# Performance work log

Measured on AMD Instinct MI355X. Metric: run time of the kernel, lower is better.

The kernel has to match this reference:

```python
import jax, jax.numpy as jnp
import numpy as np

N, E, H, C = 100000, 1600000, 64, 40

def _mlp(h, w1, b1, w2, b2):
    return jax.nn.relu(h @ w1 + b1) @ w2 + b2

def setup_inputs() -> dict:
    key = jax.random.key(0)
    ks = jax.random.split(key, 16)
    def w(k, shape, fan_in):
        return jax.random.normal(k, shape, jnp.float32) / np.sqrt(fan_in)
    return {
        "x": jax.random.normal(ks[0], (N, H), jnp.float32),
        "edge_index": jax.random.randint(ks[1], (2, E), 0, N, jnp.int64),
        "edge_attr": jax.random.normal(ks[2], (E, 1), jnp.float32),
        # edge_mlp: Linear(1,H) -> ReLU -> Linear(H,H)
        "e_w1": w(ks[3], (1, H), 1), "e_b1": jnp.zeros((H,), jnp.float32),
        "e_w2": w(ks[4], (H, H), H), "e_b2": jnp.zeros((H,), jnp.float32),
        # conv1 update MLP + eps
        "eps1": jnp.zeros((), jnp.float32),
        "m1_w1": w(ks[5], (H, H), H), "m1_b1": jnp.zeros((H,), jnp.float32),
        "m1_w2": w(ks[6], (H, H), H), "m1_b2": jnp.zeros((H,), jnp.float32),
        # conv2 update MLP + eps
        "eps2": jnp.zeros((), jnp.float32),
        "m2_w1": w(ks[7], (H, H), H), "m2_b1": jnp.zeros((H,), jnp.float32),
        "m2_w2": w(ks[8], (H, H), H), "m2_b2": jnp.zeros((H,), jnp.float32),
        # classifier
        "lin_w": w(ks[9], (H, C), H), "lin_b": jnp.zeros((C,), jnp.float32),
    }

def reference(x, edge_index, edge_attr, e_w1, e_b1, e_w2, e_b2,
              eps1, m1_w1, m1_b1, m1_w2, m1_b2,
              eps2, m2_w1, m2_b1, m2_w2, m2_b2, lin_w, lin_b):
    n = x.shape[0]
    src, dst = edge_index[0], edge_index[1]
    edge_emb = _mlp(edge_attr, e_w1, e_b1, e_w2, e_b2)  # [E, H]

    def gine_conv(h, eps, w1, b1, w2, b2):
        msg = jax.nn.relu(h[src] + edge_emb)                 # gather + fuse  [E, H]
        aggr = jax.ops.segment_sum(msg, dst, num_segments=n) # scatter-add   [N, H]
        return _mlp((1.0 + eps) * h + aggr, w1, b1, w2, b2)

    h = jax.nn.relu(gine_conv(x, eps1, m1_w1, m1_b1, m1_w2, m1_b2))
    # dropout is identity in eval mode
    h = jax.nn.relu(gine_conv(h, eps2, m2_w1, m2_b1, m2_w2, m2_b2))
    return jax.nn.log_softmax(h @ lin_w + lin_b, axis=1)
```

## Files before the change

### kernel.cpp

```cpp
#include <hip/hip_runtime.h>
#include <hip/hip_bf16.h>
#include <stdint.h>


typedef unsigned int uint32;
typedef unsigned short ushort16;
typedef __attribute__((ext_vector_type(8))) short bf16x8;
typedef __attribute__((ext_vector_type(4))) float f32x4;

#define BKT_SHIFT 9
#define BKT_SIZE 512
#define BKT_MASK 511
#define BSPLIT 4

static __device__ __forceinline__ unsigned short f2bf(float f) {
  __hip_bfloat16 h = __float2bfloat16(f);
  return *reinterpret_cast<unsigned short*>(&h);
}
static __device__ __forceinline__ float bf2f(unsigned short u) {
  return __uint_as_float(((uint32)u) << 16);
}

static __device__ __forceinline__ bool detect_is64(const uint32* ei, int E, int tid, int* sflag) {
  if (tid < 64) {
    int lim = (E < 64) ? E : 64;
    int nz = (tid < lim) ? (ei[2 * (size_t)tid + 1] != 0u) : 0;
    nz = __any(nz);
    if (tid == 0) *sflag = !nz;
  }
  __syncthreads();
  return *sflag != 0;
}

__global__ __launch_bounds__(256) void k_setup_cast_count(
    const float* __restrict__ w1, const float* __restrict__ b1,
    const float* __restrict__ w2, const float* __restrict__ b2,
    float* __restrict__ tsS, float2* __restrict__ ABp,
    const float* __restrict__ xin, ushort16* __restrict__ xb, int n4,
    const uint32* __restrict__ ei, int* __restrict__ hist1, int E, int KB) {
  __shared__ float w2s[64 * 64];
  __shared__ float b2s[64];
  __shared__ float w1s[64], b1s[64], ts[64];
  __shared__ int rs[64], ms[64], vs[64];
  __shared__ int h[1024];
  __shared__ int sIs64;
  const int tid = threadIdx.x;
  const int CB = (n4 + 255) >> 8;
  if (blockIdx.x >= (uint32)(65 + CB)) {
    const int b = blockIdx.x - (65 + CB);
    for (int i = tid; i < 1024; i += 256) h[i] = 0;
    bool is64 = detect_is64(ei, E, tid, &sIs64);
    for (int i = b * 256 + tid; i < E; i += KB * 256) {
      int dst = is64 ? (int)ei[2 * ((size_t)E + i)] : (int)ei[(size_t)E + i];
      atomicAdd(&h[dst >> BKT_SHIFT], 1);
    }
    __syncthreads();
    for (int i = tid; i < 1024; i += 256)
      if (h[i]) atomicAdd(&hist1[i], h[i]);
    return;
  }
  if (blockIdx.x >= 65) {
    int i = (blockIdx.x - 65) * 256 + tid;
    if (i < n4) {
      float4 v = ((const float4*)xin)[i];
      ushort4 o;
      o.x = f2bf(v.x); o.y = f2bf(v.y); o.z = f2bf(v.z); o.w = f2bf(v.w);
      ((ushort4*)xb)[i] = o;
    }
    return;
  }
  const int p = blockIdx.x;
  {
    const float4* g4 = (const float4*)w2;
    float4* s4 = (float4*)w2s;
    for (int i = tid; i < 64 * 16; i += 256) s4[i] = g4[i];
    if (tid < 64) b2s[tid] = b2[tid];
  }
  if (tid < 64) {
    float w = w1[tid], b = b1[tid];
    w1s[tid] = w; b1s[tid] = b;
    int v = (w != 0.0f);
    vs[tid] = v;
    ts[tid] = v ? (-b / w) : 0.0f;
  }
  __syncthreads();
  if (tid < 64) {
    float tk = ts[tid];
    int r = 0, m = 0;
    for (int k = 0; k < 64; ++k) if (vs[k]) { r += (ts[k] < tk) ? 1 : 0; m += (ts[k] == tk) ? 1 : 0; }
    rs[tid] = r; ms[tid] = m;
    if (p == 0) {
      int pos;
      if (vs[tid]) {
        int c = 0;
        for (int j = 0; j < 64; ++j)
          if (vs[j] && (ts[j] < tk || (ts[j] == tk && j < tid))) c++;
        pos = c;
      } else {
        int c = 0;
        for (int j = 0; j < 64; ++j) if (vs[j]) c++;
        for (int j = 0; j < tid; ++j) if (!vs[j]) c++;
        pos = c;
      }
      tsS[pos] = vs[tid] ? tk : __builtin_inff();
    }
  }
  __syncthreads();
  if (tid < 64) {
    const int j = tid;
    float accA = 0.0f, accB = b2s[j];
    for (int k = 0; k < 64; ++k) {
      bool act;
      if (vs[k]) act = (w1s[k] > 0.0f) ? (p >= rs[k] + ms[k]) : (p <= rs[k]);
      else       act = (b1s[k] > 0.0f);
      if (act) { float wv = w2s[k * 64 + j]; accA = fmaf(w1s[k], wv, accA); accB = fmaf(b1s[k], wv, accB); }
    }
    ABp[p * 64 + j] = make_float2(accA, accB);
  }
}

static __device__ __forceinline__ int scan_hist(const int* __restrict__ hist1,
                                                int* bo, int* psum, int tid) {
  int v0 = hist1[tid * 4 + 0], v1 = hist1[tid * 4 + 1];
  int v2 = hist1[tid * 4 + 2], v3 = hist1[tid * 4 + 3];
  int sum = v0 + v1 + v2 + v3;
  psum[tid] = sum;
  __syncthreads();
  for (int d = 1; d < 256; d <<= 1) {
    int add = (tid >= d) ? psum[tid - d] : 0;
    __syncthreads();
    psum[tid] += add;
    __syncthreads();
  }
  int run = psum[tid] - sum;
  bo[tid * 4 + 0] = run; run += v0;
  bo[tid * 4 + 1] = run; run += v1;
  bo[tid * 4 + 2] = run; run += v2;
  bo[tid * 4 + 3] = run; run += v3;
  int total = psum[255];
  __syncthreads();
  return total;
}

__global__ __launch_bounds__(256) void k_bpart(
    const uint32* __restrict__ ei, const float* __restrict__ ea,
    const float* __restrict__ tsSg, const int* __restrict__ hist1,
    int* __restrict__ bCur,
    int2* __restrict__ stage, unsigned short* __restrict__ dstw, int E) {
  __shared__ int cnt[1024];
  __shared__ int bo[1024];
  __shared__ int psum[256];
  __shared__ float tss[64];
  __shared__ int sIs64;
  __shared__ int2 sspay[2048];
  __shared__ uint32 ssmeta[2048];
  const int tid = threadIdx.x;
  for (int i = tid; i < 1024; i += 256) cnt[i] = 0;
  if (tid >= 64 && tid < 128) tss[tid - 64] = tsSg[tid - 64];
  bool is64 = detect_is64(ei, E, tid, &sIs64);
  scan_hist(hist1, bo, psum, tid);
  const int base0 = blockIdx.x * 2048;
  int dstv[8], srcv[8], rk[8];
  float av[8];
#pragma unroll
  for (int e = 0; e < 8; ++e) {
    int idx = base0 + e * 256 + tid;
    if (idx < E) {
      int src, dst;
      if (is64) { src = (int)ei[2 * (size_t)idx]; dst = (int)ei[2 * ((size_t)E + idx)]; }
      else      { src = (int)ei[(size_t)idx];     dst = (int)ei[(size_t)E + idx]; }
      dstv[e] = dst; srcv[e] = src; av[e] = ea[idx];
      rk[e] = atomicAdd(&cnt[dst >> BKT_SHIFT], 1);
    } else dstv[e] = -1;
  }
  __syncthreads();
  for (int b = tid; b < 1024; b += 256) {
    int c = cnt[b];
    if (c) bo[b] = bo[b] + atomicAdd(&bCur[b], c);
  }
  int v0 = cnt[tid * 4 + 0], v1 = cnt[tid * 4 + 1];
  int v2 = cnt[tid * 4 + 2], v3 = cnt[tid * 4 + 3];
  int lsum = v0 + v1 + v2 + v3;
  __syncthreads();
  psum[tid] = lsum;
  __syncthreads();
  for (int d = 1; d < 256; d <<= 1) {
    int add = (tid >= d) ? psum[tid - d] : 0;
    __syncthreads();
    psum[tid] += add;
    __syncthreads();
  }
  int lrun = psum[tid] - lsum;
  cnt[tid * 4 + 0] = lrun; lrun += v0;
  cnt[tid * 4 + 1] = lrun; lrun += v1;
  cnt[tid * 4 + 2] = lrun; lrun += v2;
  cnt[tid * 4 + 3] = lrun;
  const int totloc = psum[255];
  __syncthreads();
#pragma unroll
  for (int e = 0; e < 8; ++e) {
    if (dstv[e] < 0) continue;
    float a = av[e];
    int p = 0;
#pragma unroll
    for (int s = 32; s > 0; s >>= 1) if (tss[p + s - 1] < a) p += s;
    if (tss[p] < a) ++p;
    const int b = dstv[e] >> BKT_SHIFT;
    const int slot = cnt[b] + rk[e];
    const int gd = bo[b] + rk[e];
    sspay[slot] = make_int2(srcv[e] | (p << 20), __float_as_int(a));
    ssmeta[slot] = (uint32)gd | ((uint32)(dstv[e] & BKT_MASK) << 21);
  }
  __syncthreads();
  for (int j = tid; j < totloc; j += 256) {
    uint32 m = ssmeta[j];
    int gd = (int)(m & 0x1FFFFFu);
    stage[gd] = sspay[j];
    dstw[gd] = (unsigned short)(m >> 21);
  }
}

__global__ __launch_bounds__(256) void k_blocal(
    const int* __restrict__ hist1, const int2* __restrict__ stage,
    const unsigned short* __restrict__ dstw,
    int* __restrict__ offs, int2* __restrict__ pay, int N) {
  __shared__ int bo[1024];
  __shared__ int psum[256];
  __shared__ int h[512], cur[512], ps2[256];
  const int tid = threadIdx.x;
  const int b = blockIdx.x >> 2;
  const int sub = blockIdx.x & 3;
  const int nbkt = (int)gridDim.x >> 2;
  int Etot = scan_hist(hist1, bo, psum, tid);
  const int s = bo[b];
  const int e2 = (b == nbkt - 1) ? Etot : bo[b + 1];
  if (b == 0 && sub == 0 && tid == 0) offs[N] = Etot;
  h[tid] = 0; h[tid + 256] = 0;
  __syncthreads();
  for (int j = s + tid; j < e2; j += 256) atomicAdd(&h[dstw[j]], 1);
  __syncthreads();
  int a0 = h[2 * tid], a1 = h[2 * tid + 1];
  ps2[tid] = a0 + a1;
  __syncthreads();
  for (int d = 1; d < 256; d <<= 1) {
    int add = (tid >= d) ? ps2[tid - d] : 0;
    __syncthreads();
    ps2[tid] += add;
    __syncthreads();
  }
  int ex = s + ps2[tid] - (a0 + a1);
  cur[2 * tid] = ex;
  cur[2 * tid + 1] = ex + a0;
  {
    int local = 2 * tid;
    if ((local >> 7) == sub) {
      int nd0 = b * BKT_SIZE + local;
      if (nd0 < N) offs[nd0] = ex;
      if (nd0 + 1 < N) offs[nd0 + 1] = ex + a0;
    }
  }
  __syncthreads();
  const int lo = sub << 7, hi = lo + 128;
  for (int j = s + tid; j < e2; j += 256) {
    int d = dstw[j];
    if (d >= lo && d < hi) {
      int pos = atomicAdd(&cur[d], 1);
      pay[pos] = stage[j];
    }
  }
}

#define EDGE8_LOAD(ib, qx, av)                                   \
  _Pragma("unroll")                                              \
  for (int t = 0; t < 8; ++t) {                                  \
    int2 q_ = pay[(ib) + t];                                     \
    qx[t] = (uint32)__builtin_amdgcn_readfirstlane(q_.x);        \
    av[t] = __uint_as_float((uint32)__builtin_amdgcn_readfirstlane(q_.y)); \
  }

#define EDGE8_GATHER(qx, xv, ab)                                 \
  _Pragma("unroll")                                              \
  for (int t = 0; t < 8; ++t) {                                  \
    xv[t] = bf2f(xb[(size_t)(qx[t] & 0xFFFFFu) * 64u + lane]);   \
    ab[t] = ABs[(qx[t] >> 20) * 64u + lane];                     \
  }

#define EDGE8_ACC(av, xv, ab, acc)                               \
  _Pragma("unroll")                                              \
  for (int t = 0; t < 8; ++t)                                    \
    acc += fmaxf(fmaf(av[t], ab[t].x, ab[t].y) + xv[t], 0.0f);

#define EDGE1(ib, acc) do {                                      \
    int2 q_ = pay[(ib)];                                         \
    uint32 qx_ = (uint32)__builtin_amdgcn_readfirstlane(q_.x);   \
    float av_ = __uint_as_float((uint32)__builtin_amdgcn_readfirstlane(q_.y)); \
    float xv_ = bf2f(xb[(size_t)(qx_ & 0xFFFFFu) * 64u + lane]); \
    float2 ab_ = ABs[(qx_ >> 20) * 64u + lane];                  \
    acc += fmaxf(fmaf(av_, ab_.x, ab_.y) + xv_, 0.0f);           \
  } while (0)

__global__ __launch_bounds__(512, 8) void k_conv(
    const unsigned short* __restrict__ xb,
    const int* __restrict__ offs, const int2* __restrict__ pay,
    const float2* __restrict__ ABp, const float* __restrict__ epsp,
    unsigned short* __restrict__ uout, int n) {
  __shared__ float2 ABs[65 * 64];
  {
    const float4* g4 = (const float4*)ABp;
    float4* s4 = (float4*)ABs;
    for (int i = threadIdx.x; i < 65 * 32; i += 512) s4[i] = g4[i];
  }
  __syncthreads();
  const int lane = threadIdx.x & 63;
  const int wid = __builtin_amdgcn_readfirstlane((int)(threadIdx.x >> 6));
  const float scale = 1.0f + epsp[0];
  const int npair = (n + 1) >> 1;
  for (int w = blockIdx.x * 8 + wid; w < npair; w += gridDim.x * 8) {
    const int ndA = __builtin_amdgcn_readfirstlane(w * 2);
    const bool hasB = (ndA + 1) < n;
    const int sA = offs[ndA];
    const int eA = offs[ndA + 1];
    const int eB = hasB ? offs[ndA + 2] : eA;
    float accA = 0.0f, accB = 0.0f;
    int iA = sA, iB = eA;
    while (iA + 7 < eA && iB + 7 < eB) {
      const int ia = __builtin_amdgcn_readfirstlane(iA);
      const int ib = __builtin_amdgcn_readfirstlane(iB);
      uint32 qxA[8], qxB[8];
      float avA[8], avB[8];
      EDGE8_LOAD(ia, qxA, avA);
      EDGE8_LOAD(ib, qxB, avB);
      float xvA[8], xvB[8];
      float2 abA[8], abB[8];
      EDGE8_GATHER(qxA, xvA, abA);
      EDGE8_GATHER(qxB, xvB, abB);
      EDGE8_ACC(avA, xvA, abA, accA);
      EDGE8_ACC(avB, xvB, abB, accB);
      iA += 8; iB += 8;
    }
    while (iA + 7 < eA) {
      const int ia = __builtin_amdgcn_readfirstlane(iA);
      uint32 qx[8]; float av[8];
      EDGE8_LOAD(ia, qx, av);
      float xv[8]; float2 ab[8];
      EDGE8_GATHER(qx, xv, ab);
      EDGE8_ACC(av, xv, ab, accA);
      iA += 8;
    }
    while (iB + 7 < eB) {
      const int ib = __builtin_amdgcn_readfirstlane(iB);
      uint32 qx[8]; float av[8];
      EDGE8_LOAD(ib, qx, av);
      float xv[8]; float2 ab[8];
      EDGE8_GATHER(qx, xv, ab);
      EDGE8_ACC(av, xv, ab, accB);
      iB += 8;
    }
    while (iA < eA && iB < eB) {
      const int ia = __builtin_amdgcn_readfirstlane(iA);
      const int ib = __builtin_amdgcn_readfirstlane(iB);
      int2 qa = pay[ia];
      int2 qb = pay[ib];
      uint32 qxa = (uint32)__builtin_amdgcn_readfirstlane(qa.x);
      float ava = __uint_as_float((uint32)__builtin_amdgcn_readfirstlane(qa.y));
      uint32 qxb = (uint32)__builtin_amdgcn_readfirstlane(qb.x);
      float avb = __uint_as_float((uint32)__builtin_amdgcn_readfirstlane(qb.y));
      float xva = bf2f(xb[(size_t)(qxa & 0xFFFFFu) * 64u + lane]);
      float xvb = bf2f(xb[(size_t)(qxb & 0xFFFFFu) * 64u + lane]);
      float2 aba = ABs[(qxa >> 20) * 64u + lane];
      float2 abb = ABs[(qxb >> 20) * 64u + lane];
      accA += fmaxf(fmaf(ava, aba.x, aba.y) + xva, 0.0f);
      accB += fmaxf(fmaf(avb, abb.x, abb.y) + xvb, 0.0f);
      ++iA; ++iB;
    }
    while (iA < eA) { EDGE1(__builtin_amdgcn_readfirstlane(iA), accA); ++iA; }
    while (iB < eB) { EDGE1(__builtin_amdgcn_readfirstlane(iB), accB); ++iB; }
    float xsA = bf2f(xb[(size_t)ndA * 64 + lane]);
    uout[(size_t)ndA * 64 + lane] = f2bf(fmaf(scale, xsA, accA));
    if (hasB) {
      float xsB = bf2f(xb[((size_t)ndA + 1) * 64 + lane]);
      uout[((size_t)ndA + 1) * 64 + lane] = f2bf(fmaf(scale, xsB, accB));
    }
  }
}

template <int OUTW>
static __device__ __forceinline__ bf16x8 load_bfrag(const float* __restrict__ W,
                                                    int hh, int q, int ncol, bool valid) {
  bf16x8 f;
#pragma unroll
  for (int j = 0; j < 8; ++j) {
    int k = hh * 32 + q * 8 + j;
    f[j] = valid ? (short)f2bf(W[k * OUTW + ncol]) : (short)0;
  }
  return f;
}

#define MFMA_BF16(A, B, C) __builtin_amdgcn_mfma_f32_16x16x32_bf16((A), (B), (C), 0, 0, 0)

__global__ __launch_bounds__(256) void k_mlp1(
    const unsigned short* __restrict__ uin, unsigned short* __restrict__ houtb,
    const float* __restrict__ W1, const float* __restrict__ B1,
    const float* __restrict__ W2, const float* __restrict__ B2, int n) {
  __shared__ unsigned short T[4][16 * 72];
  const int lane = threadIdx.x & 63;
  const int wid = threadIdx.x >> 6;
  const int cl = lane & 15;
  const int q = lane >> 4;
  bf16x8 w1f[4][2], w2f[4][2];
  float b1v[4], b2v[4];
#pragma unroll
  for (int t = 0; t < 4; ++t) {
#pragma unroll
    for (int hh = 0; hh < 2; ++hh) {
      w1f[t][hh] = load_bfrag<64>(W1, hh, q, t * 16 + cl, true);
      w2f[t][hh] = load_bfrag<64>(W2, hh, q, t * 16 + cl, true);
    }
    b1v[t] = B1[t * 16 + cl];
    b2v[t] = B2[t * 16 + cl];
  }
  unsigned short* Tw = T[wid];
  for (int node0 = blockIdx.x * 64 + wid * 16; node0 < n; node0 += gridDim.x * 64) {
    const unsigned short* ub = uin + (size_t)(node0 + cl) * 64;
    bf16x8 au0 = *(const bf16x8*)(ub + q * 8);
    bf16x8 au1 = *(const bf16x8*)(ub + 32 + q * 8);
#pragma unroll
    for (int t = 0; t < 4; ++t) {
      f32x4 acc = {b1v[t], b1v[t], b1v[t], b1v[t]};
      acc = MFMA_BF16(au0, w1f[t][0], acc);
      acc = MFMA_BF16(au1, w1f[t][1], acc);
#pragma unroll
      for (int r = 0; r < 4; ++r)
        Tw[(q * 4 + r) * 72 + t * 16 + cl] = f2bf(fmaxf(acc[r], 0.0f));
    }
    bf16x8 ah0 = *(const bf16x8*)&Tw[cl * 72 + q * 8];
    bf16x8 ah1 = *(const bf16x8*)&Tw[cl * 72 + 32 + q * 8];
#pragma unroll
    for (int t = 0; t < 4; ++t) {
      f32x4 acc = {b2v[t], b2v[t], b2v[t], b2v[t]};
      acc = MFMA_BF16(ah0, w2f[t][0], acc);
      acc = MFMA_BF16(ah1, w2f[t][1], acc);
#pragma unroll
      for (int r = 0; r < 4; ++r)
        Tw[(q * 4 + r) * 72 + t * 16 + cl] = f2bf(fmaxf(acc[r], 0.0f));
    }
    int m2 = lane >> 2, pt = lane & 3;
    if (node0 + m2 < n) {
      bf16x8 c0 = *(const bf16x8*)&Tw[m2 * 72 + pt * 16];
      bf16x8 c1 = *(const bf16x8*)&Tw[m2 * 72 + pt * 16 + 8];
      unsigned short* ob = houtb + (size_t)(node0 + m2) * 64 + pt * 16;
      *(bf16x8*)ob = c0;
      *(bf16x8*)(ob + 8) = c1;
    }
  }
}

__global__ __launch_bounds__(256) void k_mlp_cls(
    const unsigned short* __restrict__ uin,
    const float* __restrict__ W1, const float* __restrict__ B1,
    const float* __restrict__ W2, const float* __restrict__ B2,
    const float* __restrict__ LW, const float* __restrict__ LB,
    float* __restrict__ out, int n) {
  __shared__ unsigned short T[4][16 * 72];
  __shared__ float L[4][16 * 52];
  const int lane = threadIdx.x & 63;
  const int wid = threadIdx.x >> 6;
  const int cl = lane & 15;
  const int q = lane >> 4;
  bf16x8 w1f[4][2], w2f[4][2], lwf[3][2];
  float b1v[4], b2v[4], lbv[3];
#pragma unroll
  for (int t = 0; t < 4; ++t) {
#pragma unroll
    for (int hh = 0; hh < 2; ++hh) {
      w1f[t][hh] = load_bfrag<64>(W1, hh, q, t * 16 + cl, true);
      w2f[t][hh] = load_bfrag<64>(W2, hh, q, t * 16 + cl, true);
    }
    b1v[t] = B1[t * 16 + cl];
    b2v[t] = B2[t * 16 + cl];
  }
#pragma unroll
  for (int t = 0; t < 3; ++t) {
    bool valid = (t * 16 + cl) < 40;
#pragma unroll
    for (int hh = 0; hh < 2; ++hh)
      lwf[t][hh] = load_bfrag<40>(LW, hh, q, valid ? (t * 16 + cl) : 0, valid);
    lbv[t] = valid ? LB[t * 16 + cl] : 0.0f;
  }
  unsigned short* Tw = T[wid];
  float* Lw = L[wid];
  for (int node0 = blockIdx.x * 64 + wid * 16; node0 < n; node0 += gridDim.x * 64) {
    const unsigned short* ub = uin + (size_t)(node0 + cl) * 64;
    bf16x8 au0 = *(const bf16x8*)(ub + q * 8);
    bf16x8 au1 = *(const bf16x8*)(ub + 32 + q * 8);
#pragma unroll
    for (int t = 0; t < 4; ++t) {
      f32x4 acc = {b1v[t], b1v[t], b1v[t], b1v[t]};
      acc = MFMA_BF16(au0, w1f[t][0], acc);
      acc = MFMA_BF16(au1, w1f[t][1], acc);
#pragma unroll
      for (int r = 0; r < 4; ++r)
        Tw[(q * 4 + r) * 72 + t * 16 + cl] = f2bf(fmaxf(acc[r], 0.0f));
    }
    bf16x8 ah0 = *(const bf16x8*)&Tw[cl * 72 + q * 8];
    bf16x8 ah1 = *(const bf16x8*)&Tw[cl * 72 + 32 + q * 8];
#pragma unroll
    for (int t = 0; t < 4; ++t) {
      f32x4 acc = {b2v[t], b2v[t], b2v[t], b2v[t]};
      acc = MFMA_BF16(ah0, w2f[t][0], acc);
      acc = MFMA_BF16(ah1, w2f[t][1], acc);
#pragma unroll
      for (int r = 0; r < 4; ++r)
        Tw[(q * 4 + r) * 72 + t * 16 + cl] = f2bf(fmaxf(acc[r], 0.0f));
    }
    bf16x8 g0 = *(const bf16x8*)&Tw[cl * 72 + q * 8];
    bf16x8 g1 = *(const bf16x8*)&Tw[cl * 72 + 32 + q * 8];
#pragma unroll
    for (int t = 0; t < 3; ++t) {
      f32x4 acc = {lbv[t], lbv[t], lbv[t], lbv[t]};
      acc = MFMA_BF16(g0, lwf[t][0], acc);
      acc = MFMA_BF16(g1, lwf[t][1], acc);
#pragma unroll
      for (int r = 0; r < 4; ++r)
        Lw[(q * 4 + r) * 52 + t * 16 + cl] = acc[r];
    }
    int m3 = lane >> 2, j3 = lane & 3;
    float lg[10];
#pragma unroll
    for (int i = 0; i < 10; ++i) lg[i] = Lw[m3 * 52 + j3 * 10 + i];
    float mx = lg[0];
#pragma unroll
    for (int i = 1; i < 10; ++i) mx = fmaxf(mx, lg[i]);
    mx = fmaxf(mx, __shfl_xor(mx, 1));
    mx = fmaxf(mx, __shfl_xor(mx, 2));
    float se = 0.0f;
#pragma unroll
    for (int i = 0; i < 10; ++i) se += __expf(lg[i] - mx);
    se += __shfl_xor(se, 1);
    se += __shfl_xor(se, 2);
    float lse = mx + __logf(se);
    if (node0 + m3 < n) {
      float* o = out + (size_t)(node0 + m3) * 40 + j3 * 10;
#pragma unroll
      for (int i = 0; i < 10; ++i) o[i] = lg[i] - lse;
    }
  }
}

extern "C" void kernel_launch(void* const* d_in, const int* in_sizes, int n_in,
                              void* d_out, int out_size, void* d_ws, size_t ws_size,
                              hipStream_t stream) {
  (void)n_in; (void)out_size; (void)ws_size;
  const float* x     = (const float*)d_in[0];
  const uint32* ei   = (const uint32*)d_in[1];
  const float* eattr = (const float*)d_in[2];
  const float* e_w1 = (const float*)d_in[3];
  const float* e_b1 = (const float*)d_in[4];
  const float* e_w2 = (const float*)d_in[5];
  const float* e_b2 = (const float*)d_in[6];
  const float* eps1 = (const float*)d_in[7];
  const float* m1w1 = (const float*)d_in[8];
  const float* m1b1 = (const float*)d_in[9];
  const float* m1w2 = (const float*)d_in[10];
  const float* m1b2 = (const float*)d_in[11];
  const float* eps2 = (const float*)d_in[12];
  const float* m2w1 = (const float*)d_in[13];
  const float* m2b1 = (const float*)d_in[14];
  const float* m2w2 = (const float*)d_in[15];
  const float* m2b2 = (const float*)d_in[16];
  const float* linw = (const float*)d_in[17];
  const float* linb = (const float*)d_in[18];

  const int N = in_sizes[0] / 64;
  const int E = in_sizes[1] / 2;
  const int NBKT = (N + BKT_SIZE - 1) >> BKT_SHIFT;

  char* ws = (char*)d_ws;
  size_t off = 0;
  auto alloc = [&](size_t bytes, size_t align) {
    off = (off + align - 1) & ~(align - 1);
    size_t r = off; off += bytes; return r;
  };
  size_t oT    = alloc(64 * 4, 64);
  size_t oAB   = alloc(65 * 64 * 8, 64);
  size_t oHC   = alloc(2048 * 4, 128);
  size_t oOffs = alloc(((size_t)N + 1) * 4, 128);
  size_t oPay  = alloc((size_t)E * 8, 256);
  size_t oXb   = alloc((size_t)N * 64 * 2 + 32768, 256);
  size_t oU    = alloc((size_t)N * 64 * 2 + 32768, 1024);
  size_t oStg  = alloc((size_t)E * 8, 256);
  size_t oDw   = alloc((size_t)E * 2, 256);

  float*  tsS  = (float*)(ws + oT);
  float2* ABp  = (float2*)(ws + oAB);
  int*    h1   = (int*)(ws + oHC);
  int*    bCur = (int*)(ws + oHC + 1024 * 4);
  int*    offs = (int*)(ws + oOffs);
  int2*   pay  = (int2*)(ws + oPay);
  ushort16* xb = (ushort16*)(ws + oXb);
  ushort16* ubuf = (ushort16*)(ws + oU);
  int2*   stage = (int2*)(ws + oStg);
  unsigned short* dstw = (unsigned short*)(ws + oDw);

  hipMemsetAsync(ws + oHC, 0, 2048 * 4, stream);

  const int n4 = N * 64 / 4;
  const int CB = (n4 + 255) / 256;
  const int PB = (E + 2047) / 2048;
  const int KB = 1024;
  const int MB = (N + 127) / 128;

  k_setup_cast_count<<<65 + CB + KB, 256, 0, stream>>>(
      e_w1, e_b1, e_w2, e_b2, tsS, ABp, x, xb, n4, ei, h1, E, KB);
  k_bpart<<<PB, 256, 0, stream>>>(ei, eattr, tsS, h1, bCur, stage, dstw, E);
  k_blocal<<<NBKT * BSPLIT, 256, 0, stream>>>(h1, stage, dstw, offs, pay, N);
  k_conv<<<1024, 512, 0, stream>>>((const unsigned short*)xb, offs, pay, ABp, eps1, ubuf, N);
  k_mlp1<<<MB, 256, 0, stream>>>((const unsigned short*)ubuf, (unsigned short*)xb,
                                 m1w1, m1b1, m1w2, m1b2, N);
  k_conv<<<1024, 512, 0, stream>>>((const unsigned short*)xb, offs, pay, ABp, eps2, ubuf, N);
  k_mlp_cls<<<MB, 256, 0, stream>>>((const unsigned short*)ubuf,
                                    m2w1, m2b1, m2w2, m2b2, linw, linb,
                                    (float*)d_out, N);
}
```

Before: 318.4 us.

## Split conv launches into two node-range halves and defer edge-table LDS reads

```diff
diff --git a/kernel.cpp b/kernel.cpp
--- a/kernel.cpp
+++ b/kernel.cpp
@@ -278,17 +278,17 @@
     av[t] = __uint_as_float((uint32)__builtin_amdgcn_readfirstlane(q_.y)); \
   }
 
-#define EDGE8_GATHER(qx, xv, ab)                                 \
+#define EDGE8_GATHERX(qx, xv)                                    \
+  _Pragma("unroll")                                              \
+  for (int t = 0; t < 8; ++t)                                    \
+    xv[t] = bf2f(xb[(size_t)(qx[t] & 0xFFFFFu) * 64u + lane]);
+
+#define EDGE8_ACC(qx, av, xv, acc)                               \
   _Pragma("unroll")                                              \
   for (int t = 0; t < 8; ++t) {                                  \
-    xv[t] = bf2f(xb[(size_t)(qx[t] & 0xFFFFFu) * 64u + lane]);   \
-    ab[t] = ABs[(qx[t] >> 20) * 64u + lane];                     \
-  }
-
-#define EDGE8_ACC(av, xv, ab, acc)                               \
-  _Pragma("unroll")                                              \
-  for (int t = 0; t < 8; ++t)                                    \
-    acc += fmaxf(fmaf(av[t], ab[t].x, ab[t].y) + xv[t], 0.0f);
+    float2 ab_ = ABs[(qx[t] >> 20) * 64u + lane];                \
+    acc += fmaxf(fmaf(av[t], ab_.x, ab_.y) + xv[t], 0.0f);       \
+  }
 
 #define EDGE1(ib, acc) do {                                      \
     int2 q_ = pay[(ib)];                                         \
@@ -303,7 +303,7 @@
     const unsigned short* __restrict__ xb,
     const int* __restrict__ offs, const int2* __restrict__ pay,
     const float2* __restrict__ ABp, const float* __restrict__ epsp,
-    unsigned short* __restrict__ uout, int n) {
+    unsigned short* __restrict__ uout, int n, int p0, int p1) {
   __shared__ float2 ABs[65 * 64];
   {
     const float4* g4 = (const float4*)ABp;
@@ -314,8 +314,7 @@
   const int lane = threadIdx.x & 63;
   const int wid = __builtin_amdgcn_readfirstlane((int)(threadIdx.x >> 6));
   const float scale = 1.0f + epsp[0];
-  const int npair = (n + 1) >> 1;
-  for (int w = blockIdx.x * 8 + wid; w < npair; w += gridDim.x * 8) {
+  for (int w = p0 + blockIdx.x * 8 + wid; w < p1; w += gridDim.x * 8) {
     const int ndA = __builtin_amdgcn_readfirstlane(w * 2);
     const bool hasB = (ndA + 1) < n;
     const int sA = offs[ndA];
@@ -331,29 +330,28 @@
       EDGE8_LOAD(ia, qxA, avA);
       EDGE8_LOAD(ib, qxB, avB);
       float xvA[8], xvB[8];
-      float2 abA[8], abB[8];
-      EDGE8_GATHER(qxA, xvA, abA);
-      EDGE8_GATHER(qxB, xvB, abB);
-      EDGE8_ACC(avA, xvA, abA, accA);
-      EDGE8_ACC(avB, xvB, abB, accB);
+      EDGE8_GATHERX(qxA, xvA);
+      EDGE8_GATHERX(qxB, xvB);
+      EDGE8_ACC(qxA, avA, xvA, accA);
+      EDGE8_ACC(qxB, avB, xvB, accB);
       iA += 8; iB += 8;
     }
     while (iA + 7 < eA) {
       const int ia = __builtin_amdgcn_readfirstlane(iA);
       uint32 qx[8]; float av[8];
       EDGE8_LOAD(ia, qx, av);
-      float xv[8]; float2 ab[8];
-      EDGE8_GATHER(qx, xv, ab);
-      EDGE8_ACC(av, xv, ab, accA);
+      float xv[8];
+      EDGE8_GATHERX(qx, xv);
+      EDGE8_ACC(qx, av, xv, accA);
       iA += 8;
     }
     while (iB + 7 < eB) {
       const int ib = __builtin_amdgcn_readfirstlane(iB);
       uint32 qx[8]; float av[8];
       EDGE8_LOAD(ib, qx, av);
-      float xv[8]; float2 ab[8];
-      EDGE8_GATHER(qx, xv, ab);
-      EDGE8_ACC(av, xv, ab, accB);
+      float xv[8];
+      EDGE8_GATHERX(qx, xv);
+      EDGE8_ACC(qx, av, xv, accB);
       iB += 8;
     }
     while (iA < eA && iB < eB) {
@@ -609,15 +607,23 @@
   const int PB = (E + 2047) / 2048;
   const int KB = 1024;
   const int MB = (N + 127) / 128;
+  const int npair = (N + 1) / 2;
+  const int nph = (npair + 1) / 2;
 
   k_setup_cast_count<<<65 + CB + KB, 256, 0, stream>>>(
       e_w1, e_b1, e_w2, e_b2, tsS, ABp, x, xb, n4, ei, h1, E, KB);
   k_bpart<<<PB, 256, 0, stream>>>(ei, eattr, tsS, h1, bCur, stage, dstw, E);
   k_blocal<<<NBKT * BSPLIT, 256, 0, stream>>>(h1, stage, dstw, offs, pay, N);
-  k_conv<<<1024, 512, 0, stream>>>((const unsigned short*)xb, offs, pay, ABp, eps1, ubuf, N);
+  k_conv<<<1024, 512, 0, stream>>>((const unsigned short*)xb, offs, pay, ABp, eps1,
+                                   (unsigned short*)ubuf, N, 0, nph);
+  k_conv<<<1024, 512, 0, stream>>>((const unsigned short*)xb, offs, pay, ABp, eps1,
+                                   (unsigned short*)ubuf, N, nph, npair);
   k_mlp1<<<MB, 256, 0, stream>>>((const unsigned short*)ubuf, (unsigned short*)xb,
                                  m1w1, m1b1, m1w2, m1b2, N);
-  k_conv<<<1024, 512, 0, stream>>>((const unsigned short*)xb, offs, pay, ABp, eps2, ubuf, N);
+  k_conv<<<1024, 512, 0, stream>>>((const unsigned short*)xb, offs, pay, ABp, eps2,
+                                   (unsigned short*)ubuf, N, 0, nph);
+  k_conv<<<1024, 512, 0, stream>>>((const unsigned short*)xb, offs, pay, ABp, eps2,
+                                   (unsigned short*)ubuf, N, nph, npair);
   k_mlp_cls<<<MB, 256, 0, stream>>>((const unsigned short*)ubuf,
                                     m2w1, m2b1, m2w2, m2b2, linw, linb,
                                     (float*)d_out, N);
```

New measurement: 333.0 us. 4.6% more time.
